# Optimization experiments

Measured on AMD Instinct MI355X. Metric: run time of the kernel, lower is better.

Reference implementation:

```python
import jax, jax.numpy as jnp
import numpy as np

B, D, E, NF, FD, H = 8192, 1024, 6, 32, 32, 256
MINK, MAXK = 1, 4

def _lin(a, w, b):
    return a @ w.T + b

def setup_inputs():
    key = jax.random.key(0)
    it = iter(jax.random.split(key, 60))
    def nrm(shape, s=0.02):
        return jax.random.normal(next(it), shape, jnp.float32) * s
    z = lambda *s: jnp.zeros(s, jnp.float32)
    return dict(
        x=jax.random.normal(next(it), (B, D), jnp.float32),
        esp_patterns=nrm((E, D), 1.0),
        sim_w1=nrm((D // 2, D)), sim_b1=z(D // 2),
        sim_w2=nrm((E, D // 2)), sim_b2=z(E),
        rout_w1=nrm((D // 2, D + E)), rout_b1=z(D // 2),
        rout_w2=nrm((E, D // 2)), rout_b2=z(E),
        kpred_w1=nrm((16, 6)), kpred_b1=z(16),
        kpred_w2=nrm((1, 16)), kpred_b2=z(1),
        sp_v_w=nrm((D, D)), sp_v_b=z(D),
        sp_o_w=nrm((D, D)), sp_o_b=z(D),
        sp_q1_w=nrm((D, D)), sp_q1_b=z(D),
        sp_q2_w=nrm((D, D)), sp_q2_b=z(D),
        de_w1=nrm((H, D)), de_b1=z(H),
        de_w2=nrm((D, H)), de_b2=z(D),
        de_g_w=nrm((D, D)), de_g_b=z(D),
        cf_in_w=nrm((3 * FD, FD)), cf_in_b=z(3 * FD),
        cf_o_w=nrm((FD, FD)), cf_o_b=z(FD),
        cf_f_w=nrm((FD, FD)), cf_f_b=z(FD),
        hf_w1=nrm((H, D)), hf_b1=z(H),
        hf_w2=nrm((D, H)), hf_b2=z(D),
        tc_w=nrm((4, 1, 3), 0.2), tc_b=z(4),
        tf_w=nrm((1, 4), 0.2), tf_b=z(1),
        lt_w1=nrm((H, D)), lt_b1=z(H),
        lt_w2=nrm((D, H)), lt_b2=z(D),
        op_w=nrm((D, D)), op_b=z(D),
    )

def reference(x, esp_patterns, sim_w1, sim_b1, sim_w2, sim_b2, rout_w1, rout_b1, rout_w2, rout_b2,
              kpred_w1, kpred_b1, kpred_w2, kpred_b2, sp_v_w, sp_v_b, sp_o_w, sp_o_b,
              sp_q1_w, sp_q1_b, sp_q2_w, sp_q2_b, de_w1, de_b1, de_w2, de_b2, de_g_w, de_g_b,
              cf_in_w, cf_in_b, cf_o_w, cf_o_b, cf_f_w, cf_f_b, hf_w1, hf_b1, hf_w2, hf_b2,
              tc_w, tc_b, tf_w, tf_b, lt_w1, lt_b1, lt_w2, lt_b2, op_w, op_b):
    # ---- FeatureAnalyzer ----
    sparsity = (x == 0).astype(jnp.float32).mean(-1)
    var_u = jnp.var(x, axis=-1, ddof=1)            # torch default unbiased var
    magnitude = jnp.abs(x).max(-1)
    norm = jnp.linalg.norm(x, axis=-1)
    mean = x.mean(-1, keepdims=True)
    std = jnp.sqrt(var_u[:, None] + 1e-8)
    skew = (((x - mean) / std) ** 3).mean(-1)
    s_abs = -jnp.sort(-jnp.abs(x), axis=-1)        # descending
    top20 = int(0.2 * D)
    conc = s_abs[:, :top20].sum(-1) / (s_abs.sum(-1) + 1e-8)
    feats = jnp.stack([sparsity, var_u, magnitude, norm, skew, conc], -1)  # (B,6)
    # ---- IntelligentRouter ----
    spec = jax.nn.sigmoid(x @ esp_patterns.T + _lin(jax.nn.relu(_lin(x, sim_w1, sim_b1)), sim_w2, sim_b2))
    probs = jax.nn.softmax(_lin(jax.nn.relu(_lin(jnp.concatenate([x, spec], -1), rout_w1, rout_b1)), rout_w2, rout_b2), -1)
    k_ratio = jax.nn.sigmoid(_lin(jax.nn.relu(_lin(feats, kpred_w1, kpred_b1)), kpred_w2, kpred_b2))[:, 0]
    k_vals = MINK + (MAXK - MINK) * k_ratio
    k = jnp.clip(jnp.floor(jnp.median(k_vals)), MINK, MAXK).astype(jnp.int32)  # int(median) truncation
    tp, ti = jax.lax.top_k(probs, MAXK)
    gmask = jnp.arange(MAXK) < k
    gates = jax.nn.softmax(jnp.where(gmask, tp, -jnp.inf), -1)  # (B,MAXK)
    # ---- experts (eval mode: dropout = identity) ----
    # SparseQuadraticExpert: seq-len-1 MHA collapses to V->out projections
    att = _lin(_lin(x, sp_v_w, sp_v_b), sp_o_w, sp_o_b)
    e_sp = _lin(jax.nn.relu(_lin(att * x, sp_q1_w, sp_q1_b)), sp_q2_w, sp_q2_b)
    # DenseQuadraticExpert
    e_de = _lin(jax.nn.relu(_lin(x, de_w1, de_b1)), de_w2, de_b2) + jax.nn.sigmoid(_lin(x, de_g_w, de_g_b)) * x
    # CrossFieldQuadraticExpert: single-head attention over fields
    xf = x.reshape(-1, NF, FD)
    q, kk, v = jnp.split(_lin(xf, cf_in_w, cf_in_b), 3, axis=-1)
    attn = jax.nn.softmax(jnp.einsum('bqd,bkd->bqk', q, kk) / jnp.sqrt(jnp.float32(FD)), -1)
    att_f = _lin(jnp.einsum('bqk,bkd->bqd', attn, v), cf_o_w, cf_o_b)
    e_cf = _lin(att_f * xf, cf_f_w, cf_f_b).reshape(-1, D)
    # HighFreqQuadraticExpert
    filt = _lin(jnp.tanh(_lin(x, hf_w1, hf_b1)), hf_w2, hf_b2)
    e_hf = x + (filt - x) * x
    # TemporalQuadraticExpert (AdaptiveAvgPool1d(D) on length-D input == identity)
    conv = jax.nn.relu(jax.lax.conv_general_dilated(x[:, None, :], tc_w, (1,), [(1, 1)], dimension_numbers=('NCH', 'OIH', 'NCH')) + tc_b[None, :, None])
    wts = jax.nn.sigmoid(_lin(conv.transpose(0, 2, 1), tf_w, tf_b))[..., 0]  # (B,D)
    e_tp = (x * wts) * x
    # LongTailQuadraticExpert
    t = _lin(jax.nn.elu(_lin(x, lt_w1, lt_b1)), lt_w2, lt_b2)
    e_lt = jnp.sign(x) * jnp.sqrt(jnp.abs(t * x) + 1e-8)
    # ---- dispatch + combine ----
    stack = jnp.stack([e_sp, e_de, e_cf, e_hf, e_tp, e_lt], axis=1)  # (B,E,D)
    sel = jnp.take_along_axis(stack, ti[:, :, None], axis=1)         # (B,MAXK,D)
    comb = (gates[:, :, None] * sel).sum(1)
    return _lin(comb, op_w, op_b) + x  # output projection + residual; Identity norm (batch_norm=False)
```

## Files before the change

kernel.cpp:

```cpp
#include <hip/hip_runtime.h>
#include <stdint.h>

typedef unsigned short u16;
typedef __attribute__((ext_vector_type(2))) float f32x2;
typedef __attribute__((ext_vector_type(4))) float f32x4;
typedef __attribute__((ext_vector_type(4))) unsigned short u16x4;
typedef __attribute__((ext_vector_type(8))) short short8;

#define DEV static __device__ __forceinline__

DEV float bf2f(u16 u){ union{unsigned int i; float f;} v; v.i=((unsigned int)u)<<16; return v.f; }
DEV u16 f2bf(float f){ union{float f; unsigned int i;} v; v.f=f; unsigned int u=v.i;
  return (u16)((u + 0x7FFFu + ((u>>16)&1u))>>16); }
DEV float wred(float v){ for(int o=32;o;o>>=1) v += __shfl_xor(v,o); return v; }
DEV float wredmax(float v){ for(int o=32;o;o>>=1) v = fmaxf(v,__shfl_xor(v,o)); return v; }
DEV int wredi(int v){ for(int o=32;o;o>>=1) v += __shfl_xor(v,o); return v; }

DEV void gload16(const void* g, void* l){
  __builtin_amdgcn_global_load_lds((const __attribute__((address_space(1))) unsigned int*)g,
                                   (__attribute__((address_space(3))) unsigned int*)l, 16, 0, 0);
}

DEV float actf(int ACT, float v){
  if(ACT==1) return v>0.f?v:0.f;
  if(ACT==2) return 1.f/(1.f+__expf(-v));
  if(ACT==3) return tanhf(v);
  if(ACT==4) return v>0.f?v:(__expf(v)-1.f);
  return v;
}

__global__ void cvt_kernel(const float* __restrict__ s, u16* __restrict__ d, int n4){
  for(int i=blockIdx.x*blockDim.x+threadIdx.x; i<n4; i+=gridDim.x*blockDim.x){
    f32x4 v=((const f32x4*)s)[i];
    u16x4 o;
    #pragma unroll
    for(int j=0;j<4;++j) o[j]=f2bf(v[j]);
    ((u16x4*)d)[i]=o;
  }
}

__global__ void cvt6_kernel(
    const float* __restrict__ s0, const float* __restrict__ s1, const float* __restrict__ s2,
    const float* __restrict__ s3, const float* __restrict__ s4, const float* __restrict__ s5,
    u16* __restrict__ d0, u16* __restrict__ d1, u16* __restrict__ d2,
    u16* __restrict__ d3, u16* __restrict__ d4, u16* __restrict__ d5, int n4each){
  const float* ss[6]={s0,s1,s2,s3,s4,s5};
  u16* dd[6]={d0,d1,d2,d3,d4,d5};
  const int total=6*n4each;
  for(int i=blockIdx.x*blockDim.x+threadIdx.x; i<total; i+=gridDim.x*blockDim.x){
    int b=i/n4each, r=i-b*n4each;
    f32x4 v=((const f32x4*)ss[b])[r];
    u16x4 o;
    #pragma unroll
    for(int j=0;j<4;++j) o[j]=f2bf(v[j]);
    ((u16x4*)dd[b])[r]=o;
  }
}

__global__ void cvt_split(const float* __restrict__ s, u16* __restrict__ hi, u16* __restrict__ lo, int n4){
  for(int i=blockIdx.x*blockDim.x+threadIdx.x; i<n4; i+=gridDim.x*blockDim.x){
    f32x4 v=((const f32x4*)s)[i];
    u16x4 h,l;
    #pragma unroll
    for(int j=0;j<4;++j){ h[j]=f2bf(v[j]); l[j]=f2bf(v[j]-bf2f(h[j])); }
    ((u16x4*)hi)[i]=h; ((u16x4*)lo)[i]=l;
  }
}

__global__ void cvt_split_rw1(const float* __restrict__ src, u16* __restrict__ hi, u16* __restrict__ lo){
  for(int i=blockIdx.x*blockDim.x+threadIdx.x; i<512*1024; i+=gridDim.x*blockDim.x){
    int r=i>>10, c=i&1023;
    float v=src[(size_t)r*1030+c];
    u16 h=f2bf(v);
    hi[i]=h; lo[i]=f2bf(v-bf2f(h));
  }
}

__global__ void pack_rw1t(const float* __restrict__ src, float* __restrict__ dst){
  int i=blockIdx.x*blockDim.x+threadIdx.x;
  if(i<3072){
    int e=i>>9, col=i&511;
    dst[i]=src[(size_t)col*1030+1024+e];
  }
}

__global__ __launch_bounds__(256) void transpose_bf(const float* __restrict__ src, u16* __restrict__ dst){
  __shared__ float t[32][33];
  const int bx=blockIdx.x&31, by=blockIdx.x>>5;
  const int lx=threadIdx.x&31, ly=threadIdx.x>>5;
  #pragma unroll
  for(int r=0;r<4;++r)
    t[ly+8*r][lx] = src[(size_t)(by*32+ly+8*r)*1024 + bx*32+lx];
  __syncthreads();
  #pragma unroll
  for(int r=0;r<4;++r)
    dst[(size_t)(bx*32+ly+8*r)*1024 + by*32+lx] = f2bf(t[lx][ly+8*r]);
}

__global__ __launch_bounds__(256) void bias_comp(const float* __restrict__ ow, const float* __restrict__ vb,
    const float* __restrict__ ob, float* __restrict__ bc){
  const int wv=threadIdx.x>>6, lane=threadIdx.x&63;
  const int rowi=blockIdx.x*4+wv;
  float s=0.f;
  const float* wr=ow+(size_t)rowi*1024;
  #pragma unroll
  for(int j=0;j<16;++j) s+=wr[j*64+lane]*vb[j*64+lane];
  s=wred(s);
  if(lane==0) bc[rowi]=ob[rowi]+s;
}

__global__ void pack_b768(const float* __restrict__ b0, const float* __restrict__ b1,
                          const float* __restrict__ b2, float* __restrict__ o){
  int i=blockIdx.x*blockDim.x+threadIdx.x;
  if(i<256) o[i]=b0[i];
  else if(i<512) o[i]=b1[i-256];
  else if(i<768) o[i]=b2[i-512];
}

__global__ void pack_b1024(const float* __restrict__ b0, const float* __restrict__ b1, float* __restrict__ o){
  int i=blockIdx.x*blockDim.x+threadIdx.x;
  if(i<512) o[i]=b0[i];
  else if(i<1024) o[i]=b1[i-512];
}

template<int ACT, int EPI>
__global__ __launch_bounds__(256) void gemm_bt(
    const u16* __restrict__ A, const u16* __restrict__ W,
    const float* __restrict__ bias, const u16* __restrict__ auxb,
    const float* __restrict__ auxf, const float* __restrict__ wsel,
    u16* __restrict__ comb, void* __restrict__ Cv, int M, int N, int K, int lda)
{
  __shared__ __align__(16) u16 lA[128*64];
  __shared__ __align__(16) u16 lB[128*64];
  const int tid=threadIdx.x, lane=tid&63, wv=tid>>6;
  const int wr=wv>>1, wc=wv&1;
  const int gx=gridDim.x;
  const int nwg=gx*gridDim.y;
  const int flat=blockIdx.y*gx+blockIdx.x;
  const int chunk=nwg>>3;
  const int nf=(flat&7)*chunk + (flat>>3);
  const int bn=(nf%gx)*128, bm=(nf/gx)*128;
  f32x4 acc[4][4];
  #pragma unroll
  for(int m=0;m<4;++m){
    #pragma unroll
    for(int n=0;n<4;++n) acc[m][n]=(f32x4)0.f;
  }
  const int srow = wv*8 + (lane>>3);
  const int scol = (lane&7)*8;
  for(int kt=0;kt<K;kt+=64){
    #pragma unroll
    for(int i=0;i<4;++i){
      gload16(A + (size_t)(bm + i*32 + srow)*lda + kt + scol, &lA[(i*32 + wv*8)*64]);
      gload16(W + (size_t)(bn + i*32 + srow)*K + kt + scol, &lB[(i*32 + wv*8)*64]);
    }
    __syncthreads();
    #pragma unroll
    for(int kk=0;kk<2;++kk){
      const int fr=lane&15, kc=kk*32+(lane>>4)*8;
      short8 af[4], bfr[4];
      #pragma unroll
      for(int m=0;m<4;++m) af[m]=*(const short8*)&lA[(wr*64+m*16+fr)*64+kc];
      #pragma unroll
      for(int n=0;n<4;++n) bfr[n]=*(const short8*)&lB[(wc*64+n*16+fr)*64+kc];
      #pragma unroll
      for(int m=0;m<4;++m){
        #pragma unroll
        for(int n=0;n<4;++n)
          acc[m][n]=__builtin_amdgcn_mfma_f32_16x16x32_bf16(af[m],bfr[n],acc[m][n],0,0,0);
      }
    }
    __syncthreads();
  }
  const int fr=lane&15, fq=lane>>4;
  #pragma unroll
  for(int m=0;m<4;++m){
    #pragma unroll
    for(int n=0;n<4;++n){
      const int col = bn + wc*64 + n*16 + fr;
      const float bv = bias ? bias[col] : 0.f;
      #pragma unroll
      for(int j=0;j<4;++j){
        const int row = bm + wr*64 + m*16 + fq*4 + j;
        const size_t idx = (size_t)row*N+col;
        float v = acc[m][n][j] + bv;
        if(ACT==5){
          v = (col<256) ? fmaxf(v,0.f) : (col<512 ? tanhf(v) : (v>0.f?v:(__expf(v)-1.f)));
        } else v = actf(ACT, v);
        if(EPI==0){ ((u16*)Cv)[idx]=f2bf(v); }
        else if(EPI==1){ ((float*)Cv)[idx]=v; }
        else if(EPI==2){ ((u16*)Cv)[idx]=f2bf(v*bf2f(auxb[idx])); }
        else if(EPI==3){ comb[idx]=f2bf(wsel[row*6+0]*v); }
        else if(EPI==4){ comb[idx]=f2bf(bf2f(comb[idx])+wsel[row*6+1]*(v + bf2f(auxb[idx])*auxf[idx])); }
        else if(EPI==5){ float x0=bf2f(auxb[idx]); comb[idx]=f2bf(bf2f(comb[idx])+wsel[row*6+3]*(x0+(v-x0)*x0)); }
        else if(EPI==6){
          float x0=bf2f(auxb[idx]);
          float sg=(x0>0.f)?1.f:((x0<0.f)?-1.f:0.f);
          comb[idx]=f2bf(bf2f(comb[idx])+wsel[row*6+5]*sg*sqrtf(fabsf(v*x0)+1e-8f));
        }
        else { ((float*)Cv)[idx]=v+auxf[idx]; }
      }
    }
  }
}

__global__ __launch_bounds__(256) void gemm_split2(
    const u16* __restrict__ Ah, const u16* __restrict__ Al,
    const u16* __restrict__ Wh, const u16* __restrict__ Wl,
    const float* __restrict__ bias, float* __restrict__ C, int M, int N, int K)
{
  const int LDL=40;
  __shared__ __align__(16) u16 lAh[128*40], lAl[128*40], lBh[128*40], lBl[128*40];
  const int tid=threadIdx.x, lane=tid&63, wv=tid>>6;
  const int wr=wv>>1, wc=wv&1;
  const int nwg=gridDim.x;
  const int wg=(blockIdx.x%8)*(nwg/8)+blockIdx.x/8;
  const int bx=wg&7, by=wg>>3;
  const int bn=bx*128, bm=by*128;
  f32x4 acc[4][4];
  #pragma unroll
  for(int m=0;m<4;++m){
    #pragma unroll
    for(int n=0;n<4;++n) acc[m][n]=(f32x4)0.f;
  }
  const int srow=tid>>2, scol=(tid&3)*8;
  for(int kt=0;kt<K;kt+=32){
    short8 rah[2],ral[2],rbh[2],rbl[2];
    #pragma unroll
    for(int i=0;i<2;++i){
      size_t ao=(size_t)(bm+i*64+srow)*K+kt+scol;
      size_t bo=(size_t)(bn+i*64+srow)*K+kt+scol;
      rah[i]=*(const short8*)(Ah+ao); ral[i]=*(const short8*)(Al+ao);
      rbh[i]=*(const short8*)(Wh+bo); rbl[i]=*(const short8*)(Wl+bo);
    }
    __syncthreads();
    #pragma unroll
    for(int i=0;i<2;++i){
      int d=(i*64+srow)*LDL+scol;
      *(short8*)&lAh[d]=rah[i]; *(short8*)&lAl[d]=ral[i];
      *(short8*)&lBh[d]=rbh[i]; *(short8*)&lBl[d]=rbl[i];
    }
    __syncthreads();
    const int fr=lane&15, kc=(lane>>4)*8;
    short8 ah[4],al[4],bh[4],bl[4];
    #pragma unroll
    for(int m=0;m<4;++m){ int r=(wr*64+m*16+fr)*LDL+kc; ah[m]=*(const short8*)&lAh[r]; al[m]=*(const short8*)&lAl[r]; }
    #pragma unroll
    for(int n=0;n<4;++n){ int r=(wc*64+n*16+fr)*LDL+kc; bh[n]=*(const short8*)&lBh[r]; bl[n]=*(const short8*)&lBl[r]; }
    #pragma unroll
    for(int m=0;m<4;++m){
      #pragma unroll
      for(int n=0;n<4;++n){
        acc[m][n]=__builtin_amdgcn_mfma_f32_16x16x32_bf16(ah[m],bh[n],acc[m][n],0,0,0);
        acc[m][n]=__builtin_amdgcn_mfma_f32_16x16x32_bf16(ah[m],bl[n],acc[m][n],0,0,0);
        acc[m][n]=__builtin_amdgcn_mfma_f32_16x16x32_bf16(al[m],bh[n],acc[m][n],0,0,0);
      }
    }
  }
  const int fr=lane&15, fq=lane>>4;
  #pragma unroll
  for(int m=0;m<4;++m){
    #pragma unroll
    for(int n=0;n<4;++n){
      const int col = bn + wc*64 + n*16 + fr;
      const float bv = bias[col];
      #pragma unroll
      for(int j=0;j<4;++j){
        const int row = bm + wr*64 + m*16 + fq*4 + j;
        float v = acc[m][n][j] + bv;
        if(col<512) v=fmaxf(v,0.f);
        C[(size_t)row*N+col] = v;
      }
    }
  }
}

__global__ __launch_bounds__(256) void feats_kernel(const float* __restrict__ x,
    const float* __restrict__ kw1, const float* __restrict__ kb1,
    const float* __restrict__ kw2, const float* __restrict__ kb2,
    float* __restrict__ kvals, u16* __restrict__ x_hi, u16* __restrict__ x_lo)
{
  const int lane=threadIdx.x&63, wv=threadIdx.x>>6;
  const int row=blockIdx.x*4+wv;
  const float* xr=x+(size_t)row*1024;
  u16x4* hio=(u16x4*)(x_hi+(size_t)row*1024);
  u16x4* loo=(u16x4*)(x_lo+(size_t)row*1024);
  float xv[16]; unsigned int cd[16];
  float s=0.f, ss=0.f, sa=0.f, nz=0.f, amax=0.f;
  #pragma unroll
  for(int t=0;t<4;++t){
    f32x4 v=((const f32x4*)xr)[t*64+lane];
    u16x4 h,l;
    #pragma unroll
    for(int j=0;j<4;++j){
      float f=v[j];
      union{float f;unsigned int i;} c; c.f=f;
      xv[t*4+j]=f; cd[t*4+j]=c.i&0x7fffffffu;
      h[j]=f2bf(f); l[j]=f2bf(f-bf2f(h[j]));
      s+=f; ss+=f*f; float a=fabsf(f); sa+=a; amax=fmaxf(amax,a); if(f==0.f) nz+=1.f;
    }
    hio[t*64+lane]=h; loo[t*64+lane]=l;
  }
  s=wred(s); ss=wred(ss); sa=wred(sa); nz=wred(nz); amax=wredmax(amax);
  const float mean=s/1024.f;
  const float var=(ss - s*mean)/1023.f;
  const float inv=1.f/sqrtf(var+1e-8f);
  float sk=0.f;
  #pragma unroll
  for(int j=0;j<16;++j){ float z=(xv[j]-mean)*inv; sk+=z*z*z; }
  sk=wred(sk);
  unsigned int lo=0u, hi=0x7f800000u;
  while(hi-lo>1u){
    unsigned int mid=(lo+hi)>>1;
    int c=0;
    #pragma unroll
    for(int j=0;j<16;++j) c += (cd[j] >= mid);
    c=wredi(c);
    if(c>=204) lo=mid; else hi=mid;
  }
  const unsigned int T=lo;
  float sg=0.f, cg=0.f;
  #pragma unroll
  for(int j=0;j<16;++j){ if(cd[j] > T){ sg+=fabsf(xv[j]); cg+=1.f; } }
  sg=wred(sg); cg=wred(cg);
  if(lane==0){
    union{unsigned int i;float f;} tv; tv.i=T;
    float conc=(sg + (204.f-cg)*tv.f)/(sa + 1e-8f);
    float feats[6]={ nz/1024.f, var, amax, sqrtf(ss), sk/1024.f, conc };
    float out=kb2[0];
    #pragma unroll
    for(int i=0;i<16;++i){
      float hv=kb1[i];
      #pragma unroll
      for(int j=0;j<6;++j) hv+=kw1[i*6+j]*feats[j];
      hv=fmaxf(hv,0.f);
      out+=kw2[i]*hv;
    }
    kvals[row]=1.f + 3.f*(1.f/(1.f+__expf(-out)));
  }
}

__global__ __launch_bounds__(256) void median_kernel(const float* __restrict__ kvals, int* __restrict__ kint){
  __shared__ unsigned int v[8192];
  __shared__ int hist4[4*257];
  __shared__ unsigned int selT;
  __shared__ int selR;
  const int tid=threadIdx.x, lane=tid&63, wv=tid>>6;
  for(int i=tid;i<8192;i+=256){ union{float f;unsigned int u;} c; c.f=kvals[i]; v[i]=c.u; }
  __syncthreads();
  unsigned int res[2];
  for(int t=0;t<2;++t){
    int r = 8192 - (4096+t) + 1;
    unsigned int prefix=0u;
    for(int lvl=0;lvl<4;++lvl){
      const int shift=24-lvl*8;
      const unsigned int pmask = (lvl==0)?0u:(0xFFFFFFFFu<<(shift+8));
      for(int i=tid;i<4*257;i+=256) hist4[i]=0;
      __syncthreads();
      for(int i=tid;i<8192;i+=256){
        unsigned int c=v[i];
        if((c&pmask)==prefix) atomicAdd(&hist4[wv*257+((c>>shift)&0xFFu)],1);
      }
      __syncthreads();
      if(wv==0){
        int h[4]; int ls=0;
        #pragma unroll
        for(int b=0;b<4;++b){
          int bin=lane*4+b;
          h[b]=hist4[bin]+hist4[257+bin]+hist4[514+bin]+hist4[771+bin];
          ls+=h[b];
        }
        int pfx=ls;
        #pragma unroll
        for(int off=1;off<64;off<<=1){ int tt=__shfl_up(pfx,off); if(lane>=off) pfx+=tt; }
        int total=__shfl(pfx,63);
        int cgt = total - pfx;
        #pragma unroll
        for(int b=3;b>=0;--b){
          if(cgt < r && r <= cgt + h[b]){
            selT = prefix | ((unsigned int)(lane*4+b)<<shift);
            selR = r - cgt;
          }
          cgt += h[b];
        }
      }
      __syncthreads();
      prefix=selT; r=selR;
      __syncthreads();
    }
    res[t]=prefix;
  }
  if(tid==0){
    union{unsigned int u; float f;} a,b; a.u=res[0]; b.u=res[1];
    float med=0.5f*(a.f+b.f);
    int k=(int)floorf(med);
    k = k<1?1:(k>4?4:k);
    *kint=k;
  }
}

__global__ __launch_bounds__(256) void router_kernel(const float* __restrict__ x,
    const float* __restrict__ h, const float* __restrict__ esp,
    const float* __restrict__ w2s, const float* __restrict__ b2s,
    const float* __restrict__ rw1t, const float* __restrict__ w2r,
    const float* __restrict__ b2r, const int* __restrict__ kint,
    float* __restrict__ wsel)
{
  const int wv=threadIdx.x>>6, lane=threadIdx.x&63;
  const int row=blockIdx.x*4+wv;
  const float* xr=x+(size_t)row*1024;
  const float* hr=h+(size_t)row*1024;
  float xv[16], h0[8], h1[8];
  #pragma unroll
  for(int j=0;j<16;++j) xv[j]=xr[j*64+lane];
  #pragma unroll
  for(int j=0;j<8;++j){ h0[j]=hr[j*64+lane]; h1[j]=hr[512+j*64+lane]; }
  float spec[6];
  #pragma unroll
  for(int e=0;e<6;++e){
    float s=0.f;
    #pragma unroll
    for(int j=0;j<16;++j) s+=xv[j]*esp[e*1024+j*64+lane];
    #pragma unroll
    for(int j=0;j<8;++j) s+=h0[j]*w2s[e*512+j*64+lane];
    s=wred(s);
    spec[e]=1.f/(1.f+__expf(-(s+b2s[e])));
  }
  #pragma unroll
  for(int e=0;e<6;++e){
    const float se=spec[e];
    #pragma unroll
    for(int j=0;j<8;++j) h1[j]+=se*rw1t[e*512+j*64+lane];
  }
  #pragma unroll
  for(int j=0;j<8;++j) h1[j]=fmaxf(h1[j],0.f);
  float p[6];
  float m=-1e30f;
  #pragma unroll
  for(int e=0;e<6;++e){
    float s=0.f;
    #pragma unroll
    for(int j=0;j<8;++j) s+=h1[j]*w2r[e*512+j*64+lane];
    p[e]=wred(s)+b2r[e];
    m=fmaxf(m,p[e]);
  }
  float den=0.f;
  #pragma unroll
  for(int e=0;e<6;++e){ p[e]=__expf(p[e]-m); den+=p[e]; }
  float invd=1.f/den;
  #pragma unroll
  for(int e=0;e<6;++e) p[e]*=invd;
  if(lane==0){
    const int k=*kint;
    float w[6]={0,0,0,0,0,0};
    bool used[6]={false,false,false,false,false,false};
    int idx[4]; float val[4];
    #pragma unroll
    for(int j=0;j<4;++j){
      int bi=0; float bv=-1e30f;
      #pragma unroll
      for(int e=0;e<6;++e) if(!used[e] && p[e]>bv){ bv=p[e]; bi=e; }
      used[bi]=true; idx[j]=bi; val[j]=bv;
    }
    float mm=val[0], dd=0.f, g[4]={0,0,0,0};
    for(int j=0;j<k;++j){ g[j]=__expf(val[j]-mm); dd+=g[j]; }
    for(int j=0;j<k;++j) w[idx[j]]=g[j]/dd;
    float* o=&wsel[(size_t)row*6];
    o[0]=w[0]; o[1]=w[1]; o[2]=w[2]; o[3]=w[3]; o[4]=w[4]; o[5]=w[5];
  }
}

__global__ __launch_bounds__(256) void cf_kernel(const float* __restrict__ x,
    const float* __restrict__ w_in, const float* __restrict__ b_in,
    const float* __restrict__ w_o, const float* __restrict__ b_o,
    const float* __restrict__ w_f, const float* __restrict__ b_f,
    const float* __restrict__ wsel, u16* __restrict__ comb){
  __shared__ __align__(16) u16 smem[6400 + 4*6144];
  const int tid=threadIdx.x, wv=tid>>6, lane=tid&63;
  const int fr=lane&15, fq=lane>>4;
  for(int i=tid;i<5120;i+=256){
    float v=(i<3072)? w_in[i] : (i<4096? w_o[i-3072] : w_f[i-4096]);
    smem[(i>>5)*40 + (i&31)] = f2bf(v);
  }
  u16* wb   = smem + 6400 + wv*6144;
  float* xfl= (float*)wb;
  u16* bufA = wb + 2304;
  u16* bufB = bufA + 1280;
  u16* bufC = bufB + 1280;
  const int row = blockIdx.x*4 + wv;
  const float* xr = x + (size_t)row*1024;
  #pragma unroll
  for(int t=0;t<4;++t){
    f32x4 v = ((const f32x4*)xr)[t*64+lane];
    int e=(t*64+lane)*4;
    *(f32x4*)&xfl[(e>>5)*36 + (e&31)] = v;
  }
  __syncthreads();
  short8 xa[2];
  #pragma unroll
  for(int ft=0;ft<2;++ft){
    f32x4 a=*(const f32x4*)&xfl[(ft*16+fr)*36 + fq*8];
    f32x4 b=*(const f32x4*)&xfl[(ft*16+fr)*36 + fq*8 + 4];
    short8 s;
    s[0]=(short)f2bf(a[0]); s[1]=(short)f2bf(a[1]); s[2]=(short)f2bf(a[2]); s[3]=(short)f2bf(a[3]);
    s[4]=(short)f2bf(b[0]); s[5]=(short)f2bf(b[1]); s[6]=(short)f2bf(b[2]); s[7]=(short)f2bf(b[3]);
    xa[ft]=s;
  }
  f32x4 acc1[2][6];
  #pragma unroll
  for(int ct=0;ct<6;++ct){
    short8 wfrag=*(const short8*)&smem[(ct*16+fr)*40 + fq*8];
    #pragma unroll
    for(int ft=0;ft<2;++ft)
      acc1[ft][ct]=__builtin_amdgcn_mfma_f32_16x16x32_bf16(xa[ft],wfrag,(f32x4)0.f,0,0,0);
  }
  float bi[6];
  #pragma unroll
  for(int ct=0;ct<6;++ct) bi[ct]=b_in[ct*16+fr];
  #pragma unroll
  for(int ct=0;ct<6;++ct){
    #pragma unroll
    for(int ft=0;ft<2;++ft){
      #pragma unroll
      for(int j=0;j<4;++j){
        u16 h=f2bf(acc1[ft][ct][j]+bi[ct]);
        int rg=ft*16+fq*4+j, cg=ct*16+fr;
        if(cg<32)      bufA[rg*40+cg]=h;
        else if(cg<64) bufB[rg*40+(cg-32)]=h;
        else           bufC[(cg-64)*40+rg]=h;
      }
    }
  }
  __syncthreads();
  short8 qa0=*(const short8*)&bufA[fr*40+fq*8];
  short8 qa1=*(const short8*)&bufA[(16+fr)*40+fq*8];
  short8 kb0=*(const short8*)&bufB[fr*40+fq*8];
  short8 kb1=*(const short8*)&bufB[(16+fr)*40+fq*8];
  f32x4 aS[2][2];
  aS[0][0]=__builtin_amdgcn_mfma_f32_16x16x32_bf16(qa0,kb0,(f32x4)0.f,0,0,0);
  aS[0][1]=__builtin_amdgcn_mfma_f32_16x16x32_bf16(qa0,kb1,(f32x4)0.f,0,0,0);
  aS[1][0]=__builtin_amdgcn_mfma_f32_16x16x32_bf16(qa1,kb0,(f32x4)0.f,0,0,0);
  aS[1][1]=__builtin_amdgcn_mfma_f32_16x16x32_bf16(qa1,kb1,(f32x4)0.f,0,0,0);
  const float scale=0.17677669529663687f;
  #pragma unroll
  for(int rt=0;rt<2;++rt){
    #pragma unroll
    for(int j=0;j<4;++j){
      float e0=aS[rt][0][j]*scale, e1=aS[rt][1][j]*scale;
      float m=fmaxf(e0,e1);
      #pragma unroll
      for(int o=1;o<16;o<<=1) m=fmaxf(m,__shfl_xor(m,o));
      e0=__expf(e0-m); e1=__expf(e1-m);
      float den=e0+e1;
      #pragma unroll
      for(int o=1;o<16;o<<=1) den+=__shfl_xor(den,o);
      float inv=1.f/den;
      bufA[(rt*16+fq*4+j)*40 + fr]      = f2bf(e0*inv);
      bufA[(rt*16+fq*4+j)*40 + 16+fr]   = f2bf(e1*inv);
    }
  }
  __syncthreads();
  short8 pa0=*(const short8*)&bufA[fr*40+fq*8];
  short8 pa1=*(const short8*)&bufA[(16+fr)*40+fq*8];
  short8 vb0=*(const short8*)&bufC[fr*40+fq*8];
  short8 vb1=*(const short8*)&bufC[(16+fr)*40+fq*8];
  f32x4 aA[2][2];
  aA[0][0]=__builtin_amdgcn_mfma_f32_16x16x32_bf16(pa0,vb0,(f32x4)0.f,0,0,0);
  aA[0][1]=__builtin_amdgcn_mfma_f32_16x16x32_bf16(pa0,vb1,(f32x4)0.f,0,0,0);
  aA[1][0]=__builtin_amdgcn_mfma_f32_16x16x32_bf16(pa1,vb0,(f32x4)0.f,0,0,0);
  aA[1][1]=__builtin_amdgcn_mfma_f32_16x16x32_bf16(pa1,vb1,(f32x4)0.f,0,0,0);
  #pragma unroll
  for(int rt=0;rt<2;++rt)
    #pragma unroll
    for(int dt=0;dt<2;++dt)
      #pragma unroll
      for(int j=0;j<4;++j)
        bufB[(rt*16+fq*4+j)*40 + dt*16+fr]=f2bf(aA[rt][dt][j]);
  __syncthreads();
  short8 aa0=*(const short8*)&bufB[fr*40+fq*8];
  short8 aa1=*(const short8*)&bufB[(16+fr)*40+fq*8];
  short8 ob0=*(const short8*)&smem[(96+fr)*40+fq*8];
  short8 ob1=*(const short8*)&smem[(112+fr)*40+fq*8];
  f32x4 aF[2][2];
  aF[0][0]=__builtin_amdgcn_mfma_f32_16x16x32_bf16(aa0,ob0,(f32x4)0.f,0,0,0);
  aF[0][1]=__builtin_amdgcn_mfma_f32_16x16x32_bf16(aa0,ob1,(f32x4)0.f,0,0,0);
  aF[1][0]=__builtin_amdgcn_mfma_f32_16x16x32_bf16(aa1,ob0,(f32x4)0.f,0,0,0);
  aF[1][1]=__builtin_amdgcn_mfma_f32_16x16x32_bf16(aa1,ob1,(f32x4)0.f,0,0,0);
  float bo[2]={b_o[fr], b_o[16+fr]};
  #pragma unroll
  for(int rt=0;rt<2;++rt){
    #pragma unroll
    for(int dt=0;dt<2;++dt){
      #pragma unroll
      for(int j=0;j<4;++j){
        int fld=rt*16+fq*4+j, d=dt*16+fr;
        float attf=aF[rt][dt][j]+bo[dt];
        bufC[fld*40+d]=f2bf(attf*xfl[fld*36+d]);
      }
    }
  }
  __syncthreads();
  short8 pr0=*(const short8*)&bufC[fr*40+fq*8];
  short8 pr1=*(const short8*)&bufC[(16+fr)*40+fq*8];
  short8 fb0=*(const short8*)&smem[(128+fr)*40+fq*8];
  short8 fb1=*(const short8*)&smem[(144+fr)*40+fq*8];
  f32x4 aE[2][2];
  aE[0][0]=__builtin_amdgcn_mfma_f32_16x16x32_bf16(pr0,fb0,(f32x4)0.f,0,0,0);
  aE[0][1]=__builtin_amdgcn_mfma_f32_16x16x32_bf16(pr0,fb1,(f32x4)0.f,0,0,0);
  aE[1][0]=__builtin_amdgcn_mfma_f32_16x16x32_bf16(pr1,fb0,(f32x4)0.f,0,0,0);
  aE[1][1]=__builtin_amdgcn_mfma_f32_16x16x32_bf16(pr1,fb1,(f32x4)0.f,0,0,0);
  float bff[2]={b_f[fr], b_f[16+fr]};
  const float w2=wsel[row*6+2];
  u16* cb=&comb[(size_t)row*1024];
  #pragma unroll
  for(int rt=0;rt<2;++rt){
    #pragma unroll
    for(int dt=0;dt<2;++dt){
      #pragma unroll
      for(int j=0;j<4;++j){
        int fld=rt*16+fq*4+j, d=dt*16+fr;
        u16 old=cb[fld*32+d];
        cb[fld*32+d]=f2bf(bf2f(old)+w2*(aE[rt][dt][j]+bff[dt]));
      }
    }
  }
}

__global__ __launch_bounds__(256) void tp_kernel(const float* __restrict__ x,
    const float* __restrict__ wsel, const u16* __restrict__ comb,
    const float* __restrict__ tcw, const float* __restrict__ tcb,
    const float* __restrict__ tfw, const float* __restrict__ tfb,
    u16* __restrict__ obf){
  __shared__ float xs[1026];
  const int row=blockIdx.x, tid=threadIdx.x;
  f32x4 u=((const f32x4*)(x+(size_t)row*1024))[tid];
  #pragma unroll
  for(int j=0;j<4;++j) xs[1+4*tid+j]=u[j];
  if(tid==0){ xs[0]=0.f; xs[1025]=0.f; }
  __syncthreads();
  const float w4=wsel[row*6+4];
  float tc[4][3], tb[4], tf[4];
  #pragma unroll
  for(int o=0;o<4;++o){
    #pragma unroll
    for(int kh=0;kh<3;++kh) tc[o][kh]=tcw[o*3+kh];
    tb[o]=tcb[o]; tf[o]=tfw[o];
  }
  const float tfb0=tfb[0];
  u16x4 cv=((const u16x4*)(comb+(size_t)row*1024))[tid];
  u16x4 ov;
  #pragma unroll
  for(int j=0;j<4;++j){
    const int d=4*tid+j;
    float pre=tfb0;
    #pragma unroll
    for(int o=0;o<4;++o){
      float c=tb[o]+tc[o][0]*xs[d]+tc[o][1]*xs[d+1]+tc[o][2]*xs[d+2];
      pre+=tf[o]*fmaxf(c,0.f);
    }
    float wt=1.f/(1.f+__expf(-pre));
    float xv=xs[1+d];
    ov[j]=f2bf(bf2f(cv[j])+w4*xv*xv*wt);
  }
  ((u16x4*)(obf+(size_t)row*1024))[tid]=ov;
}

extern "C" void kernel_launch(void* const* d_in, const int* in_sizes, int n_in,
                              void* d_out, int out_size, void* d_ws, size_t ws_size,
                              hipStream_t stream)
{
  const float* x     =(const float*)d_in[0];
  const float* esp   =(const float*)d_in[1];
  const float* sim_w1=(const float*)d_in[2],  *sim_b1=(const float*)d_in[3];
  const float* sim_w2=(const float*)d_in[4],  *sim_b2=(const float*)d_in[5];
  const float* rout_w1=(const float*)d_in[6], *rout_b1=(const float*)d_in[7];
  const float* rout_w2=(const float*)d_in[8], *rout_b2=(const float*)d_in[9];
  const float* kw1=(const float*)d_in[10], *kb1=(const float*)d_in[11];
  const float* kw2=(const float*)d_in[12], *kb2=(const float*)d_in[13];
  const float* spv_w=(const float*)d_in[14], *spv_b=(const float*)d_in[15];
  const float* spo_w=(const float*)d_in[16], *spo_b=(const float*)d_in[17];
  const float* spq1_w=(const float*)d_in[18], *spq1_b=(const float*)d_in[19];
  const float* spq2_w=(const float*)d_in[20], *spq2_b=(const float*)d_in[21];
  const float* de_w1=(const float*)d_in[22], *de_b1=(const float*)d_in[23];
  const float* de_w2=(const float*)d_in[24], *de_b2=(const float*)d_in[25];
  const float* de_gw=(const float*)d_in[26], *de_gb=(const float*)d_in[27];
  const float* cf_inw=(const float*)d_in[28], *cf_inb=(const float*)d_in[29];
  const float* cf_ow=(const float*)d_in[30], *cf_ob=(const float*)d_in[31];
  const float* cf_fw=(const float*)d_in[32], *cf_fb=(const float*)d_in[33];
  const float* hf_w1=(const float*)d_in[34], *hf_b1=(const float*)d_in[35];
  const float* hf_w2=(const float*)d_in[36], *hf_b2=(const float*)d_in[37];
  const float* tc_w=(const float*)d_in[38], *tc_b=(const float*)d_in[39];
  const float* tf_w=(const float*)d_in[40], *tf_b=(const float*)d_in[41];
  const float* lt_w1=(const float*)d_in[42], *lt_b1=(const float*)d_in[43];
  const float* lt_w2=(const float*)d_in[44], *lt_b2=(const float*)d_in[45];
  const float* op_w=(const float*)d_in[46], *op_b=(const float*)d_in[47];
  float* out=(float*)d_out;
  (void)in_sizes; (void)n_in; (void)out_size; (void)ws_size;

  constexpr int NB=8192;
  const size_t BD=(size_t)NB*1024;
  char* base=(char*)d_ws; size_t off=0;
  auto carve=[&](size_t n)->void*{ void* q=base+off; off+=(n+255)&~(size_t)255; return q; };
  u16*  comb =(u16*)carve(BD*2);
  u16*  bufA =(u16*)carve(BD*2);
  u16*  bufB =(u16*)carve(BD*2);
  u16*  x_hi =(u16*)carve(BD*2);
  u16*  x_lo =(u16*)carve(BD*2);
  float* h1024=(float*)carve(BD*4);
  u16*  h768 =(u16*)carve((size_t)NB*768*2);
  u16* w1024h=(u16*)carve((size_t)1024*1024*2);
  u16* w1024l=(u16*)carve((size_t)1024*1024*2);
  u16* spv_bf =(u16*)carve((size_t)1024*1024*2);
  u16* spo_bf =(u16*)carve((size_t)1024*1024*2);
  u16* spq1_bf=(u16*)carve((size_t)1024*1024*2);
  u16* spq2_bf=(u16*)carve((size_t)1024*1024*2);
  u16* w768_bf=(u16*)carve((size_t)768*1024*2);
  u16* dew2_bf=(u16*)carve((size_t)1024*256*2);
  u16* degw_bf=(u16*)carve((size_t)1024*1024*2);
  u16* hfw2_bf=(u16*)carve((size_t)1024*256*2);
  u16* ltw2_bf=(u16*)carve((size_t)1024*256*2);
  u16* opw_bf =(u16*)carve((size_t)1024*1024*2);
  u16* spvT_bf=(u16*)carve((size_t)1024*1024*2);
  float* bc   =(float*)carve((size_t)1024*4);
  float* b768 =(float*)carve((size_t)768*4);
  float* b1024=(float*)carve((size_t)1024*4);
  float* rw1t =(float*)carve((size_t)3072*4);
  float* wsel=(float*)carve((size_t)NB*6*4);
  float* kvals=(float*)carve((size_t)NB*4);
  int*   kint=(int*)carve(256);

  const dim3 blk(256);
  auto cgrid=[&](int n4)->dim3{ int g=(n4+255)/256; return dim3(g>2048?2048:g); };

  feats_kernel<<<dim3(2048),blk,0,stream>>>(x, kw1,kb1,kw2,kb2, kvals, x_hi, x_lo);
  median_kernel<<<dim3(1),blk,0,stream>>>(kvals, kint);

  cvt_split<<<cgrid(131072),blk,0,stream>>>(sim_w1, w1024h, w1024l, 131072);
  cvt_split_rw1<<<cgrid(131072),blk,0,stream>>>(rout_w1, w1024h+524288, w1024l+524288);
  cvt6_kernel<<<cgrid(6*262144),blk,0,stream>>>(spv_w,spo_w,spq1_w,spq2_w,de_gw,op_w,
                                                spv_bf,spo_bf,spq1_bf,spq2_bf,degw_bf,opw_bf, 262144);
  cvt6_kernel<<<cgrid(6*65536),blk,0,stream>>>(de_w1,de_w2,hf_w1,hf_w2,lt_w1,lt_w2,
                                               w768_bf,dew2_bf,w768_bf+262144,hfw2_bf,w768_bf+524288,ltw2_bf, 65536);
  transpose_bf<<<dim3(1024),blk,0,stream>>>(spv_w, spvT_bf);
  bias_comp<<<dim3(256),blk,0,stream>>>(spo_w, spv_b, spo_b, bc);
  pack_b768<<<dim3(3),blk,0,stream>>>(de_b1, hf_b1, lt_b1, b768);
  pack_b1024<<<dim3(4),blk,0,stream>>>(sim_b1, rout_b1, b1024);
  pack_rw1t<<<dim3(12),blk,0,stream>>>(rout_w1, rw1t);

  gemm_split2<<<dim3(512),blk,0,stream>>>(x_hi,x_lo, w1024h,w1024l, b1024, h1024, NB,1024,1024);
  router_kernel<<<dim3(2048),blk,0,stream>>>(x, h1024, esp, sim_w2, sim_b2, rw1t, rout_w2, rout_b2, kint, wsel);

  gemm_bt<0,1><<<dim3(8,8),blk,0,stream>>>(spo_bf, spvT_bf, nullptr, nullptr, nullptr, nullptr, nullptr, h1024, 1024,1024,1024,1024);
  cvt_kernel<<<cgrid(262144),blk,0,stream>>>(h1024, spv_bf, 262144);

  gemm_bt<0,2><<<dim3(8,64),blk,0,stream>>>(x_hi, spv_bf, bc, x_hi, nullptr, nullptr, nullptr, bufB, NB,1024,1024,1024);
  gemm_bt<1,0><<<dim3(8,64),blk,0,stream>>>(bufB, spq1_bf, spq1_b, nullptr, nullptr, nullptr, nullptr, bufA, NB,1024,1024,1024);
  gemm_bt<0,3><<<dim3(8,64),blk,0,stream>>>(bufA, spq2_bf, spq2_b, nullptr, nullptr, wsel, comb, nullptr, NB,1024,1024,1024);

  gemm_bt<5,0><<<dim3(6,64),blk,0,stream>>>(x_hi, w768_bf, b768, nullptr, nullptr, nullptr, nullptr, h768, NB,768,1024,1024);

  gemm_bt<2,0><<<dim3(8,64),blk,0,stream>>>(x_hi, degw_bf, de_gb, nullptr, nullptr, nullptr, nullptr, bufB, NB,1024,1024,1024);
  gemm_bt<0,4><<<dim3(8,64),blk,0,stream>>>(h768, dew2_bf, de_b2, bufB, x, wsel, comb, nullptr, NB,1024,256,768);

  cf_kernel<<<dim3(2048),blk,0,stream>>>(x, cf_inw, cf_inb, cf_ow, cf_ob, cf_fw, cf_fb, wsel, comb);

  gemm_bt<0,5><<<dim3(8,64),blk,0,stream>>>(h768+256, hfw2_bf, hf_b2, x_hi, nullptr, wsel, comb, nullptr, NB,1024,256,768);

  gemm_bt<0,6><<<dim3(8,64),blk,0,stream>>>(h768+512, ltw2_bf, lt_b2, x_hi, nullptr, wsel, comb, nullptr, NB,1024,256,768);

  tp_kernel<<<dim3(NB),blk,0,stream>>>(x, wsel, comb, tc_w, tc_b, tf_w, tf_b, bufB);

  gemm_bt<0,7><<<dim3(8,64),blk,0,stream>>>(bufB, opw_bf, op_b, nullptr, x, nullptr, nullptr, out, NB,1024,1024,1024);
}
```

Before: 559.8 us.

## Fuse the three x-input GEMMs into one wide GEMM and merge small pack kernels

```diff
diff --git a/kernel.cpp b/kernel.cpp
--- a/kernel.cpp
+++ b/kernel.cpp
@@ -76,14 +76,6 @@
   }
 }
 
-__global__ void pack_rw1t(const float* __restrict__ src, float* __restrict__ dst){
-  int i=blockIdx.x*blockDim.x+threadIdx.x;
-  if(i<3072){
-    int e=i>>9, col=i&511;
-    dst[i]=src[(size_t)col*1030+1024+e];
-  }
-}
-
 __global__ __launch_bounds__(256) void transpose_bf(const float* __restrict__ src, u16* __restrict__ dst){
   __shared__ float t[32][33];
   const int bx=blockIdx.x&31, by=blockIdx.x>>5;
@@ -97,30 +89,42 @@
     dst[(size_t)(bx*32+ly+8*r)*1024 + by*32+lx] = f2bf(t[lx][ly+8*r]);
 }
 
-__global__ __launch_bounds__(256) void bias_comp(const float* __restrict__ ow, const float* __restrict__ vb,
-    const float* __restrict__ ob, float* __restrict__ bc){
-  const int wv=threadIdx.x>>6, lane=threadIdx.x&63;
-  const int rowi=blockIdx.x*4+wv;
-  float s=0.f;
-  const float* wr=ow+(size_t)rowi*1024;
-  #pragma unroll
-  for(int j=0;j<16;++j) s+=wr[j*64+lane]*vb[j*64+lane];
-  s=wred(s);
-  if(lane==0) bc[rowi]=ob[rowi]+s;
-}
-
-__global__ void pack_b768(const float* __restrict__ b0, const float* __restrict__ b1,
-                          const float* __restrict__ b2, float* __restrict__ o){
-  int i=blockIdx.x*blockDim.x+threadIdx.x;
-  if(i<256) o[i]=b0[i];
-  else if(i<512) o[i]=b1[i-256];
-  else if(i<768) o[i]=b2[i-512];
-}
-
-__global__ void pack_b1024(const float* __restrict__ b0, const float* __restrict__ b1, float* __restrict__ o){
-  int i=blockIdx.x*blockDim.x+threadIdx.x;
-  if(i<512) o[i]=b0[i];
-  else if(i<1024) o[i]=b1[i-512];
+__global__ __launch_bounds__(256) void small_pack(
+    const float* __restrict__ spo_w, const float* __restrict__ spv_b, const float* __restrict__ spo_b,
+    const float* __restrict__ de_gb, const float* __restrict__ de_b1,
+    const float* __restrict__ hf_b1, const float* __restrict__ lt_b1,
+    const float* __restrict__ sim_b1, const float* __restrict__ rout_b1,
+    const float* __restrict__ rout_w1,
+    float* __restrict__ b2816, float* __restrict__ b1024, float* __restrict__ rw1t)
+{
+  const int b=blockIdx.x, tid=threadIdx.x;
+  if(b<256){
+    const int wv=tid>>6, lane=tid&63;
+    const int rowi=b*4+wv;
+    float s=0.f;
+    const float* wr=spo_w+(size_t)rowi*1024;
+    #pragma unroll
+    for(int j=0;j<16;++j) s+=wr[j*64+lane]*spv_b[j*64+lane];
+    s=wred(s);
+    if(lane==0) b2816[rowi]=spo_b[rowi]+s;
+  } else if(b==256){
+    for(int i=tid;i<1024;i+=256) b2816[1024+i]=de_gb[i];
+    for(int i=tid;i<768;i+=256){
+      float v = (i<256)? de_b1[i] : (i<512? hf_b1[i-256] : lt_b1[i-512]);
+      b2816[2048+i]=v;
+    }
+  } else if(b==257){
+    for(int i=tid;i<1024;i+=256) b1024[i]= (i<512)? sim_b1[i] : rout_b1[i-512];
+  } else {
+    int base=(b-258)*1536;
+    for(int t=tid;t<1536;t+=256){
+      int i=base+t;
+      if(i<3072){
+        int e=i>>9, col=i&511;
+        rw1t[i]=rout_w1[(size_t)col*1030+1024+e];
+      }
+    }
+  }
 }
 
 template<int ACT, int EPI>
@@ -128,7 +132,8 @@
     const u16* __restrict__ A, const u16* __restrict__ W,
     const float* __restrict__ bias, const u16* __restrict__ auxb,
     const float* __restrict__ auxf, const float* __restrict__ wsel,
-    u16* __restrict__ comb, void* __restrict__ Cv, int M, int N, int K, int lda)
+    u16* __restrict__ comb, void* __restrict__ Cv, u16* __restrict__ auxg,
+    int M, int N, int K, int lda)
 {
   __shared__ __align__(16) u16 lA[128*64];
   __shared__ __align__(16) u16 lB[128*64];
@@ -198,7 +203,20 @@
           float sg=(x0>0.f)?1.f:((x0<0.f)?-1.f:0.f);
           comb[idx]=f2bf(bf2f(comb[idx])+wsel[row*6+5]*sg*sqrtf(fabsf(v*x0)+1e-8f));
         }
-        else { ((float*)Cv)[idx]=v+auxf[idx]; }
+        else if(EPI==7){ ((float*)Cv)[idx]=v+auxf[idx]; }
+        else {
+          if(col<1024){
+            size_t i1=(size_t)row*1024+col;
+            ((u16*)Cv)[i1]=f2bf(v*bf2f(auxb[i1]));
+          } else if(col<2048){
+            size_t i1=(size_t)row*1024+(col-1024);
+            comb[i1]=f2bf(1.f/(1.f+__expf(-v)));
+          } else {
+            int c7=col-2048;
+            float a = (c7<256) ? fmaxf(v,0.f) : (c7<512 ? tanhf(v) : (v>0.f?v:(__expf(v)-1.f)));
+            auxg[(size_t)row*768+c7]=f2bf(a);
+          }
+        }
       }
     }
   }
@@ -704,25 +722,23 @@
   u16*  comb =(u16*)carve(BD*2);
   u16*  bufA =(u16*)carve(BD*2);
   u16*  bufB =(u16*)carve(BD*2);
+  u16*  gate =(u16*)carve(BD*2);
   u16*  x_hi =(u16*)carve(BD*2);
   u16*  x_lo =(u16*)carve(BD*2);
   float* h1024=(float*)carve(BD*4);
   u16*  h768 =(u16*)carve((size_t)NB*768*2);
   u16* w1024h=(u16*)carve((size_t)1024*1024*2);
   u16* w1024l=(u16*)carve((size_t)1024*1024*2);
-  u16* spv_bf =(u16*)carve((size_t)1024*1024*2);
+  u16* wBig  =(u16*)carve((size_t)2816*1024*2);
   u16* spo_bf =(u16*)carve((size_t)1024*1024*2);
   u16* spq1_bf=(u16*)carve((size_t)1024*1024*2);
   u16* spq2_bf=(u16*)carve((size_t)1024*1024*2);
-  u16* w768_bf=(u16*)carve((size_t)768*1024*2);
   u16* dew2_bf=(u16*)carve((size_t)1024*256*2);
-  u16* degw_bf=(u16*)carve((size_t)1024*1024*2);
   u16* hfw2_bf=(u16*)carve((size_t)1024*256*2);
   u16* ltw2_bf=(u16*)carve((size_t)1024*256*2);
   u16* opw_bf =(u16*)carve((size_t)1024*1024*2);
   u16* spvT_bf=(u16*)carve((size_t)1024*1024*2);
-  float* bc   =(float*)carve((size_t)1024*4);
-  float* b768 =(float*)carve((size_t)768*4);
+  float* b2816=(float*)carve((size_t)2816*4);
   float* b1024=(float*)carve((size_t)1024*4);
   float* rw1t =(float*)carve((size_t)3072*4);
   float* wsel=(float*)carve((size_t)NB*6*4);
@@ -737,38 +753,34 @@
 
   cvt_split<<<cgrid(131072),blk,0,stream>>>(sim_w1, w1024h, w1024l, 131072);
   cvt_split_rw1<<<cgrid(131072),blk,0,stream>>>(rout_w1, w1024h+524288, w1024l+524288);
-  cvt6_kernel<<<cgrid(6*262144),blk,0,stream>>>(spv_w,spo_w,spq1_w,spq2_w,de_gw,op_w,
-                                                spv_bf,spo_bf,spq1_bf,spq2_bf,degw_bf,opw_bf, 262144);
+  cvt6_kernel<<<cgrid(6*262144),blk,0,stream>>>(spo_w,spq1_w,spq2_w,de_gw,op_w,spv_w,
+                                                spo_bf,spq1_bf,spq2_bf,wBig+1048576,opw_bf,spvT_bf, 262144);
   cvt6_kernel<<<cgrid(6*65536),blk,0,stream>>>(de_w1,de_w2,hf_w1,hf_w2,lt_w1,lt_w2,
-                                               w768_bf,dew2_bf,w768_bf+262144,hfw2_bf,w768_bf+524288,ltw2_bf, 65536);
+                                               wBig+2097152,dew2_bf,wBig+2097152+262144,hfw2_bf,wBig+2097152+524288,ltw2_bf, 65536);
   transpose_bf<<<dim3(1024),blk,0,stream>>>(spv_w, spvT_bf);
-  bias_comp<<<dim3(256),blk,0,stream>>>(spo_w, spv_b, spo_b, bc);
-  pack_b768<<<dim3(3),blk,0,stream>>>(de_b1, hf_b1, lt_b1, b768);
-  pack_b1024<<<dim3(4),blk,0,stream>>>(sim_b1, rout_b1, b1024);
-  pack_rw1t<<<dim3(12),blk,0,stream>>>(rout_w1, rw1t);
+  small_pack<<<dim3(260),blk,0,stream>>>(spo_w, spv_b, spo_b, de_gb, de_b1, hf_b1, lt_b1,
+                                         sim_b1, rout_b1, rout_w1, b2816, b1024, rw1t);
 
   gemm_split2<<<dim3(512),blk,0,stream>>>(x_hi,x_lo, w1024h,w1024l, b1024, h1024, NB,1024,1024);
   router_kernel<<<dim3(2048),blk,0,stream>>>(x, h1024, esp, sim_w2, sim_b2, rw1t, rout_w2, rout_b2, kint, wsel);
 
-  gemm_bt<0,1><<<dim3(8,8),blk,0,stream>>>(spo_bf, spvT_bf, nullptr, nullptr, nullptr, nullptr, nullptr, h1024, 1024,1024,1024,1024);
-  cvt_kernel<<<cgrid(262144),blk,0,stream>>>(h1024, spv_bf, 262144);
-
-  gemm_bt<0,2><<<dim3(8,64),blk,0,stream>>>(x_hi, spv_bf, bc, x_hi, nullptr, nullptr, nullptr, bufB, NB,1024,1024,1024);
-  gemm_bt<1,0><<<dim3(8,64),blk,0,stream>>>(bufB, spq1_bf, spq1_b, nullptr, nullptr, nullptr, nullptr, bufA, NB,1024,1024,1024);
-  gemm_bt<0,3><<<dim3(8,64),blk,0,stream>>>(bufA, spq2_bf, spq2_b, nullptr, nullptr, wsel, comb, nullptr, NB,1024,1024,1024);
-
-  gemm_bt<5,0><<<dim3(6,64),blk,0,stream>>>(x_hi, w768_bf, b768, nullptr, nullptr, nullptr, nullptr, h768, NB,768,1024,1024);
-
-  gemm_bt<2,0><<<dim3(8,64),blk,0,stream>>>(x_hi, degw_bf, de_gb, nullptr, nullptr, nullptr, nullptr, bufB, NB,1024,1024,1024);
-  gemm_bt<0,4><<<dim3(8,64),blk,0,stream>>>(h768, dew2_bf, de_b2, bufB, x, wsel, comb, nullptr, NB,1024,256,768);
+  gemm_bt<0,1><<<dim3(8,8),blk,0,stream>>>(spo_bf, spvT_bf, nullptr, nullptr, nullptr, nullptr, nullptr, h1024, nullptr, 1024,1024,1024,1024);
+  cvt_kernel<<<cgrid(262144),blk,0,stream>>>(h1024, wBig, 262144);
+
+  gemm_bt<0,8><<<dim3(22,64),blk,0,stream>>>(x_hi, wBig, b2816, x_hi, nullptr, nullptr, gate, bufB, h768, NB,2816,1024,1024);
+
+  gemm_bt<1,0><<<dim3(8,64),blk,0,stream>>>(bufB, spq1_bf, spq1_b, nullptr, nullptr, nullptr, nullptr, bufA, nullptr, NB,1024,1024,1024);
+  gemm_bt<0,3><<<dim3(8,64),blk,0,stream>>>(bufA, spq2_bf, spq2_b, nullptr, nullptr, wsel, comb, nullptr, nullptr, NB,1024,1024,1024);
+
+  gemm_bt<0,4><<<dim3(8,64),blk,0,stream>>>(h768, dew2_bf, de_b2, gate, x, wsel, comb, nullptr, nullptr, NB,1024,256,768);
 
   cf_kernel<<<dim3(2048),blk,0,stream>>>(x, cf_inw, cf_inb, cf_ow, cf_ob, cf_fw, cf_fb, wsel, comb);
 
-  gemm_bt<0,5><<<dim3(8,64),blk,0,stream>>>(h768+256, hfw2_bf, hf_b2, x_hi, nullptr, wsel, comb, nullptr, NB,1024,256,768);
-
-  gemm_bt<0,6><<<dim3(8,64),blk,0,stream>>>(h768+512, ltw2_bf, lt_b2, x_hi, nullptr, wsel, comb, nullptr, NB,1024,256,768);
+  gemm_bt<0,5><<<dim3(8,64),blk,0,stream>>>(h768+256, hfw2_bf, hf_b2, x_hi, nullptr, wsel, comb, nullptr, nullptr, NB,1024,256,768);
+
+  gemm_bt<0,6><<<dim3(8,64),blk,0,stream>>>(h768+512, ltw2_bf, lt_b2, x_hi, nullptr, wsel, comb, nullptr, nullptr, NB,1024,256,768);
 
   tp_kernel<<<dim3(NB),blk,0,stream>>>(x, wsel, comb, tc_w, tc_b, tf_w, tf_b, bufB);
 
-  gemm_bt<0,7><<<dim3(8,64),blk,0,stream>>>(bufB, opw_bf, op_b, nullptr, x, nullptr, nullptr, out, NB,1024,1024,1024);
-}
+  gemm_bt<0,7><<<dim3(8,64),blk,0,stream>>>(bufB, opw_bf, op_b, nullptr, x, nullptr, nullptr, out, nullptr, NB,1024,1024,1024);
+}
```

Result: slower. 572.7 us (+2.3%).
